# Optimization experiments

Hardware: AMD Instinct MI355X
Metric: run time of the kernel (lower is better)

## Reference

```python
import jax, jax.numpy as jnp
import numpy as np

EPS = 1e-6
GROUPS = 32  # min(C//4, 32) with C=256

def group_norm(x, scale, bias):
    B, H, W, C = x.shape
    g = GROUPS
    xg = x.reshape(B, H, W, g, C // g)
    mean = jnp.mean(xg, axis=(1, 2, 4), keepdims=True)
    var = jnp.var(xg, axis=(1, 2, 4), keepdims=True)
    xg = (xg - mean) * jax.lax.rsqrt(var + EPS)
    return xg.reshape(B, H, W, C) * scale + bias

def nin(x, w, b):
    return jnp.einsum('bhwc,cd->bhwd', x, w) + b

def setup_inputs() -> dict:
    key = jax.random.key(0)
    ks = jax.random.split(key, 11)
    B, H, W, C = 8, 64, 64, 256
    s = 1.0 / np.sqrt(C)
    return {
        'x': jax.random.normal(ks[0], (B, H, W, C), jnp.float32),
        'gn_scale': jnp.ones((C,), jnp.float32),
        'gn_bias': jnp.zeros((C,), jnp.float32),
        'Wq': jax.random.normal(ks[1], (C, C), jnp.float32) * s,
        'bq': jnp.zeros((C,), jnp.float32),
        'Wk': jax.random.normal(ks[2], (C, C), jnp.float32) * s,
        'bk': jnp.zeros((C,), jnp.float32),
        'Wv': jax.random.normal(ks[3], (C, C), jnp.float32) * s,
        'bv': jnp.zeros((C,), jnp.float32),
        'Wo': jax.random.normal(ks[4], (C, C), jnp.float32) * s * 0.1,
        'bo': jnp.zeros((C,), jnp.float32),
    }

def reference(x, gn_scale, gn_bias, Wq, bq, Wk, bk, Wv, bv, Wo, bo):
    B, H, W, C = x.shape
    h = group_norm(x, gn_scale, gn_bias)
    q = nin(h, Wq, bq)
    k = nin(h, Wk, bk)
    v = nin(h, Wv, bv)
    w = jnp.einsum('bhwc,bHWc->bhwHW', q, k) * (C ** -0.5)
    w = w.reshape(B, H, W, H * W)
    w = jax.nn.softmax(w, axis=-1)
    w = w.reshape(B, H, W, H, W)
    h = jnp.einsum('bhwHW,bHWc->bhwc', w, v)
    h = nin(h, Wo, bo)
    return x + h
```

## Files before the change

### kernel.cpp

```cpp
#include <hip/hip_runtime.h>
#include <stdint.h>

using short8 = __attribute__((ext_vector_type(8))) short;
using f32x4  = __attribute__((ext_vector_type(4))) float;

#define L2E 1.44269504088896f

static __device__ __forceinline__ unsigned short f2bf(float f) {
  union { float f; uint32_t u; } v; v.f = f;
  uint32_t r = v.u + 0x7fffu + ((v.u >> 16) & 1u);
  return (unsigned short)(r >> 16);
}
static __device__ __forceinline__ float bf2f(unsigned short u) {
  union { uint32_t u; float f; } v; v.u = ((uint32_t)u) << 16;
  return v.f;
}

static __device__ __forceinline__ void gload16(const unsigned short* g, unsigned short* l) {
  __builtin_amdgcn_global_load_lds(
      (const __attribute__((address_space(1))) void*)g,
      (__attribute__((address_space(3))) void*)l, 16, 0, 0);
}

static __device__ __forceinline__ float red_add_lg(float x) {
  x += __shfl_xor(x, 16);
  x += __shfl_xor(x, 32);
  return x;
}
static __device__ __forceinline__ float red_max_lg(float x) {
  x = fmaxf(x, __shfl_xor(x, 16));
  x = fmaxf(x, __shfl_xor(x, 32));
  return x;
}

__global__ __launch_bounds__(256) void prep_gn(
    const float* __restrict__ Wq, const float* __restrict__ Wk,
    const float* __restrict__ Wv, const float* __restrict__ Wo,
    const float* __restrict__ x,
    unsigned short* __restrict__ Wt, float* __restrict__ part) {
  int bid = blockIdx.x;
  int tid = threadIdx.x;
  if (bid < 1024) {
    int d = bid & 255, w = bid >> 8;
    const float* src = (w==0)?Wq:(w==1)?Wk:(w==2)?Wv:Wo;
    Wt[w*65536 + d*256 + tid] = f2bf(src[tid*256 + d]);
  } else {
    int v = bid - 1024;
    int ch = v & 63, b = v >> 6;
    float s = 0.f, q = 0.f;
    const float* p = x + ((b*4096) + ch*64)*256 + tid;
    for (int it = 0; it < 64; ++it) {
      float vv = p[it*256];
      s += vv; q += vv*vv;
    }
    s += __shfl_xor(s,1); q += __shfl_xor(q,1);
    s += __shfl_xor(s,2); q += __shfl_xor(q,2);
    s += __shfl_xor(s,4); q += __shfl_xor(q,4);
    if ((tid & 7) == 0) {
      int g = tid >> 3;
      part[((b*64 + ch)*32 + g)*2 + 0] = s;
      part[((b*64 + ch)*32 + g)*2 + 1] = q;
    }
  }
}

__global__ __launch_bounds__(256) void gn_apply(
    const float* __restrict__ x, const float* __restrict__ part,
    const float* __restrict__ sc, const float* __restrict__ bi,
    unsigned short* __restrict__ h) {
  int c = threadIdx.x, ch = blockIdx.x, b = blockIdx.y;
  int g = c >> 3;
  float s = 0.f, q = 0.f;
  for (int cc = 0; cc < 64; ++cc) {
    s += part[((b*64 + cc)*32 + g)*2 + 0];
    q += part[((b*64 + cc)*32 + g)*2 + 1];
  }
  float mean = s * (1.f/32768.f);
  float var  = q * (1.f/32768.f) - mean*mean;
  float rstd = rsqrtf(var + 1e-6f);
  float a  = rstd * sc[c];
  float d0 = bi[c] - mean * a;
  const float* p = x + ((b*4096) + ch*64)*256 + c;
  unsigned short* o = h + ((b*4096) + ch*64)*256 + c;
  for (int it = 0; it < 64; ++it)
    o[it*256] = f2bf(p[it*256] * a + d0);
}

__global__ __launch_bounds__(256) void gemm_qkvt(
    const unsigned short* __restrict__ A,
    const unsigned short* __restrict__ Wt,
    const float* __restrict__ bq,
    const float* __restrict__ bk,
    const float* __restrict__ bv,
    unsigned short* __restrict__ Qout,
    unsigned short* __restrict__ Kout,
    unsigned short* __restrict__ Vt) {
  int bid = blockIdx.x;
  int tid = threadIdx.x;
  int w = tid >> 6, l = tid & 63, lr = l & 15, lg = l >> 4;
  if (bid < 512) {
    const unsigned short* Wtq = Wt;
    const unsigned short* Wtk = Wt + 65536;
    int i0 = bid * 64;
    int j0 = w * 64;
    f32x4 accq[4][4] = {}, acck[4][4] = {};
#pragma unroll
    for (int kk = 0; kk < 8; ++kk) {
      short8 af[4], bfq[4], bfk[4];
#pragma unroll
      for (int mi = 0; mi < 4; ++mi)
        af[mi] = *(const short8*)(A + (i0 + mi*16 + lr)*256 + kk*32 + lg*8);
#pragma unroll
      for (int ni = 0; ni < 4; ++ni) {
        bfq[ni] = *(const short8*)(Wtq + (j0 + ni*16 + lr)*256 + kk*32 + lg*8);
        bfk[ni] = *(const short8*)(Wtk + (j0 + ni*16 + lr)*256 + kk*32 + lg*8);
      }
#pragma unroll
      for (int mi = 0; mi < 4; ++mi)
#pragma unroll
        for (int ni = 0; ni < 4; ++ni) {
          accq[mi][ni] = __builtin_amdgcn_mfma_f32_16x16x32_bf16(af[mi], bfq[ni], accq[mi][ni], 0,0,0);
          acck[mi][ni] = __builtin_amdgcn_mfma_f32_16x16x32_bf16(af[mi], bfk[ni], acck[mi][ni], 0,0,0);
        }
    }
#pragma unroll
    for (int mi = 0; mi < 4; ++mi) {
#pragma unroll
      for (int ni = 0; ni < 4; ++ni) {
        int j = j0 + ni*16 + lr;
#pragma unroll
        for (int r = 0; r < 4; ++r) {
          int i = i0 + mi*16 + lg*4 + r;
          Qout[i*256 + j] = f2bf((accq[mi][ni][r] + bq[j]) * 0.0625f);
          Kout[i*256 + j] = f2bf(acck[mi][ni][r] + bk[j]);
        }
      }
    }
  } else {
    const unsigned short* Wtv = Wt + 131072;
    int v = bid - 512;
    int i0 = (v & 3) * 64;
    int j0 = (v >> 2) * 256 + w * 64;
    f32x4 acc[4][4] = {};
#pragma unroll
    for (int kk = 0; kk < 8; ++kk) {
      short8 af[4], bfr[4];
#pragma unroll
      for (int mi = 0; mi < 4; ++mi)
        af[mi] = *(const short8*)(Wtv + (i0 + mi*16 + lr)*256 + kk*32 + lg*8);
#pragma unroll
      for (int ni = 0; ni < 4; ++ni)
        bfr[ni] = *(const short8*)(A + (j0 + ni*16 + lr)*256 + kk*32 + lg*8);
#pragma unroll
      for (int mi = 0; mi < 4; ++mi)
#pragma unroll
        for (int ni = 0; ni < 4; ++ni)
          acc[mi][ni] = __builtin_amdgcn_mfma_f32_16x16x32_bf16(af[mi], bfr[ni], acc[mi][ni], 0,0,0);
    }
#pragma unroll
    for (int mi = 0; mi < 4; ++mi) {
#pragma unroll
      for (int ni = 0; ni < 4; ++ni) {
        int j = j0 + ni*16 + lr;
#pragma unroll
        for (int r = 0; r < 4; ++r) {
          int i = i0 + mi*16 + lg*4 + r;
          int idx = ((j >> 12) << 20) + i*4096 + (j & 4095);
          Vt[idx] = f2bf(acc[mi][ni][r] + bv[i]);
        }
      }
    }
  }
}

__global__ __launch_bounds__(256) void gemm_bt(
    const unsigned short* __restrict__ A,
    const unsigned short* __restrict__ Bm,
    const float* __restrict__ bias_n,
    const float* __restrict__ resid,
    float* __restrict__ outp) {
  int tid = threadIdx.x;
  int w = tid >> 6, l = tid & 63, lr = l & 15, lg = l >> 4;
  int i0 = blockIdx.x * 64;
  int j0 = w * 64;
  f32x4 acc[4][4] = {};
#pragma unroll
  for (int kk = 0; kk < 8; ++kk) {
    short8 af[4], bfr[4];
#pragma unroll
    for (int mi = 0; mi < 4; ++mi)
      af[mi] = *(const short8*)(A + (i0 + mi*16 + lr)*256 + kk*32 + lg*8);
#pragma unroll
    for (int ni = 0; ni < 4; ++ni)
      bfr[ni] = *(const short8*)(Bm + (j0 + ni*16 + lr)*256 + kk*32 + lg*8);
#pragma unroll
    for (int mi = 0; mi < 4; ++mi)
#pragma unroll
      for (int ni = 0; ni < 4; ++ni)
        acc[mi][ni] = __builtin_amdgcn_mfma_f32_16x16x32_bf16(af[mi], bfr[ni], acc[mi][ni], 0,0,0);
  }
#pragma unroll
  for (int mi = 0; mi < 4; ++mi) {
#pragma unroll
    for (int ni = 0; ni < 4; ++ni) {
      int j = j0 + ni*16 + lr;
#pragma unroll
      for (int r = 0; r < 4; ++r) {
        int i = i0 + mi*16 + lg*4 + r;
        outp[i*256 + j] = acc[mi][ni][r] + bias_n[j] + resid[i*256 + j];
      }
    }
  }
}

__global__ __launch_bounds__(256) void gemm_fin(
    const unsigned short* __restrict__ P0,
    const unsigned short* __restrict__ P1,
    const float* __restrict__ stats,
    const unsigned short* __restrict__ Bm,
    const float* __restrict__ bias_n,
    const float* __restrict__ resid,
    float* __restrict__ outp) {
  int tid = threadIdx.x;
  int w = tid >> 6, l = tid & 63, lr = l & 15, lg = l >> 4;
  int i0 = blockIdx.x * 64;
  int j0 = w * 64;
  float a1m[4], a2m[4];
#pragma unroll
  for (int mi = 0; mi < 4; ++mi) {
    int row = i0 + mi*16 + lr;
    float m1 = stats[row*2 + 0],           l1 = stats[row*2 + 1];
    float m2 = stats[65536 + row*2 + 0],   l2 = stats[65536 + row*2 + 1];
    float M  = fmaxf(m1, m2);
    float a1 = __builtin_amdgcn_exp2f((m1 - M) * L2E);
    float a2 = __builtin_amdgcn_exp2f((m2 - M) * L2E);
    float inv = 1.f / (a1*l1 + a2*l2);
    a1m[mi] = a1 * inv; a2m[mi] = a2 * inv;
  }
  f32x4 acc[4][4] = {};
#pragma unroll
  for (int kk = 0; kk < 8; ++kk) {
    short8 af[4], bfr[4];
#pragma unroll
    for (int mi = 0; mi < 4; ++mi) {
      int off = (i0 + mi*16 + lr)*256 + kk*32 + lg*8;
      short8 v1 = *(const short8*)(P0 + off);
      short8 v2 = *(const short8*)(P1 + off);
      union { unsigned int u[4]; short8 s8; } pk;
#pragma unroll
      for (int e = 0; e < 4; ++e) {
        float g0 = bf2f((unsigned short)v1[2*e])   * a1m[mi] + bf2f((unsigned short)v2[2*e])   * a2m[mi];
        float g1 = bf2f((unsigned short)v1[2*e+1]) * a1m[mi] + bf2f((unsigned short)v2[2*e+1]) * a2m[mi];
        asm("v_cvt_pk_bf16_f32 %0, %1, %2" : "=v"(pk.u[e]) : "v"(g0), "v"(g1));
      }
      af[mi] = pk.s8;
    }
#pragma unroll
    for (int ni = 0; ni < 4; ++ni)
      bfr[ni] = *(const short8*)(Bm + (j0 + ni*16 + lr)*256 + kk*32 + lg*8);
#pragma unroll
    for (int mi = 0; mi < 4; ++mi)
#pragma unroll
      for (int ni = 0; ni < 4; ++ni)
        acc[mi][ni] = __builtin_amdgcn_mfma_f32_16x16x32_bf16(af[mi], bfr[ni], acc[mi][ni], 0,0,0);
  }
#pragma unroll
  for (int mi = 0; mi < 4; ++mi) {
#pragma unroll
    for (int ni = 0; ni < 4; ++ni) {
      int j = j0 + ni*16 + lr;
#pragma unroll
      for (int r = 0; r < 4; ++r) {
        int i = i0 + mi*16 + lg*4 + r;
        outp[i*256 + j] = acc[mi][ni][r] + bias_n[j] + resid[i*256 + j];
      }
    }
  }
}

static __device__ __forceinline__ void stage_kv32(
    const unsigned short* __restrict__ Kb, const unsigned short* __restrict__ Vb,
    int kt, unsigned short* dK, unsigned short* dV, int w, int l) {
#pragma unroll
  for (int i = 0; i < 4; ++i) {
    int t = (w*4 + i)*64 + l;
    int r = t >> 5, cs = t & 31;
    int cg = cs ^ (r & 7);
    gload16(Kb + (kt*32 + r)*256 + cg*8, dK + t*8);
  }
#pragma unroll
  for (int i = 0; i < 4; ++i) {
    int t = (w*4 + i)*64 + l;
    int d = t >> 2, s = t & 3;
    int sg = s ^ ((d ^ (d >> 2)) & 3);
    gload16(Vb + d*4096 + kt*32 + sg*8, dV + t*8);
  }
}

__global__ __launch_bounds__(256, 2) void attn_fwd(
    const unsigned short* __restrict__ Q,
    const unsigned short* __restrict__ Kmat,
    const unsigned short* __restrict__ Vt,
    unsigned short* __restrict__ P0,
    unsigned short* __restrict__ P1,
    float* __restrict__ stats) {
  __shared__ __align__(16) unsigned short ldsK[2][32][256];
  __shared__ __align__(16) unsigned short ldsV[2][256][32];

  int tid = threadIdx.x;
  int w = tid >> 6, l = tid & 63, lr = l & 15, lg = l >> 4;
  int b  = blockIdx.x & 7;
  int mt = (blockIdx.x >> 3) & 31;
  int ks = blockIdx.x >> 8;
  int m0 = mt*128 + w*32;
  int sw = lr & 7;
  int vsw = (lr ^ (lr >> 2)) & 3;
  int lgp = ((lg & 1) << 1) | (lg >> 1);

  const unsigned short* Kb = Kmat + b*(4096*256) + ks*(2048*256);
  const unsigned short* Vb = Vt   + (b << 20) + ks*2048;
  unsigned short* Pp = ks ? P1 : P0;

  short8 qf[2][8];
#pragma unroll
  for (int qn = 0; qn < 2; ++qn) {
    int qbase = ((b*4096) + m0 + qn*16 + lr)*256 + lg*8;
#pragma unroll
    for (int kk = 0; kk < 8; ++kk)
      qf[qn][kk] = *(const short8*)(Q + qbase + kk*32);
  }

  float mrun[2], lrun[2];
  f32x4 oacc[2][16] = {};
  mrun[0] = mrun[1] = -1e30f;
  lrun[0] = lrun[1] = 0.f;

  stage_kv32(Kb, Vb, 0, &ldsK[0][0][0], &ldsV[0][0][0], w, l);

  for (int kt = 0; kt < 64; ++kt) {
    int cur = kt & 1;
    if (kt < 63) {
      stage_kv32(Kb, Vb, kt+1, &ldsK[cur^1][0][0], &ldsV[cur^1][0][0], w, l);
      asm volatile("s_waitcnt vmcnt(8)" ::: "memory");
    } else {
      asm volatile("s_waitcnt vmcnt(0)" ::: "memory");
    }
    __builtin_amdgcn_s_barrier();
    __builtin_amdgcn_sched_barrier(0);

    const unsigned short (*Kc)[256] = ldsK[cur];
    const unsigned short (*Vc)[32]  = ldsV[cur];

    f32x4 s_[2][2];
#pragma unroll
    for (int qn = 0; qn < 2; ++qn)
#pragma unroll
      for (int kn = 0; kn < 2; ++kn) s_[qn][kn] = (f32x4){0.f,0.f,0.f,0.f};
#pragma unroll
    for (int kn = 0; kn < 2; ++kn) {
#pragma unroll
      for (int kk = 0; kk < 8; ++kk) {
        short8 kf = *(const short8*)&Kc[kn*16 + lr][((kk*4 + lg) ^ sw)*8];
        s_[0][kn] = __builtin_amdgcn_mfma_f32_16x16x32_bf16(kf, qf[0][kk], s_[0][kn], 0,0,0);
        s_[1][kn] = __builtin_amdgcn_mfma_f32_16x16x32_bf16(kf, qf[1][kk], s_[1][kn], 0,0,0);
      }
    }

    short8 pa[2];
#pragma unroll
    for (int qn = 0; qn < 2; ++qn) {
      float ma = fmaxf(fmaxf(s_[qn][0][0], s_[qn][0][1]), fmaxf(s_[qn][0][2], s_[qn][0][3]));
      float mb = fmaxf(fmaxf(s_[qn][1][0], s_[qn][1][1]), fmaxf(s_[qn][1][2], s_[qn][1][3]));
      float pmax = fmaxf(ma, mb);
      if (__any(pmax > mrun[qn] + 8.f)) {
        float mx = red_max_lg(pmax);
        float mnew = fmaxf(mrun[qn], mx);
        float alpha = __builtin_amdgcn_exp2f((mrun[qn] - mnew) * L2E);
        mrun[qn] = mnew;
        lrun[qn] *= alpha;
        float at[4];
#pragma unroll
        for (int r = 0; r < 4; ++r) at[r] = __shfl(alpha, lg*4 + r);
#pragma unroll
        for (int jt = 0; jt < 16; ++jt)
#pragma unroll
          for (int r = 0; r < 4; ++r) oacc[qn][jt][r] *= at[r];
      }
      float mL = mrun[qn] * L2E;
      float p[2][4];
#pragma unroll
      for (int kn = 0; kn < 2; ++kn)
#pragma unroll
        for (int r = 0; r < 4; ++r)
          p[kn][r] = __builtin_amdgcn_exp2f(s_[qn][kn][r]*L2E - mL);
      float t0 = (p[0][0]+p[0][1]) + (p[0][2]+p[0][3]);
      float t1 = (p[1][0]+p[1][1]) + (p[1][2]+p[1][3]);
      lrun[qn] += red_add_lg(t0 + t1);
      unsigned int X0, X1, Y0, Y1;
      asm("v_cvt_pk_bf16_f32 %0, %1, %2" : "=v"(X0) : "v"(p[0][0]), "v"(p[0][1]));
      asm("v_cvt_pk_bf16_f32 %0, %1, %2" : "=v"(X1) : "v"(p[0][2]), "v"(p[0][3]));
      asm("v_cvt_pk_bf16_f32 %0, %1, %2" : "=v"(Y0) : "v"(p[1][0]), "v"(p[1][1]));
      asm("v_cvt_pk_bf16_f32 %0, %1, %2" : "=v"(Y1) : "v"(p[1][2]), "v"(p[1][3]));
      asm("v_permlane16_swap_b32 %0, %1" : "+v"(X0), "+v"(Y0));
      asm("v_permlane16_swap_b32 %0, %1" : "+v"(X1), "+v"(Y1));
      union { unsigned int u[4]; short8 s8; } pk;
      pk.u[0] = X0; pk.u[1] = X1; pk.u[2] = Y0; pk.u[3] = Y1;
      pa[qn] = pk.s8;
    }

#pragma unroll
    for (int jt = 0; jt < 16; ++jt) {
      short8 vf = *(const short8*)&Vc[jt*16 + lr][(lgp ^ vsw)*8];
      oacc[0][jt] = __builtin_amdgcn_mfma_f32_16x16x32_bf16(pa[0], vf, oacc[0][jt], 0,0,0);
      oacc[1][jt] = __builtin_amdgcn_mfma_f32_16x16x32_bf16(pa[1], vf, oacc[1][jt], 0,0,0);
    }
    __builtin_amdgcn_sched_barrier(0);
    __builtin_amdgcn_s_barrier();
  }

  if (lg == 0) {
#pragma unroll
    for (int qn = 0; qn < 2; ++qn) {
      int row = b*4096 + m0 + qn*16 + lr;
      stats[(ks*32768 + row)*2 + 0] = mrun[qn];
      stats[(ks*32768 + row)*2 + 1] = lrun[qn];
    }
  }
#pragma unroll
  for (int qn = 0; qn < 2; ++qn) {
#pragma unroll
    for (int r = 0; r < 4; ++r) {
      int row = ((b*4096) + m0 + qn*16 + lg*4 + r)*256;
#pragma unroll
      for (int jt = 0; jt < 16; ++jt)
        Pp[row + jt*16 + lr] = f2bf(oacc[qn][jt][r]);
    }
  }
}

__global__ __launch_bounds__(256) void merge_attn(
    const unsigned short* __restrict__ P0,
    const unsigned short* __restrict__ P1,
    const float* __restrict__ stats,
    unsigned short* __restrict__ Out) {
  int tid = threadIdx.x;
  int row = blockIdx.x*8 + (tid >> 5);
  int c8  = (tid & 31) * 8;
  float m1 = stats[row*2 + 0],          l1 = stats[row*2 + 1];
  float m2 = stats[(32768 + row)*2 + 0], l2 = stats[(32768 + row)*2 + 1];
  float M  = fmaxf(m1, m2);
  float a1 = __builtin_amdgcn_exp2f((m1 - M) * L2E);
  float a2 = __builtin_amdgcn_exp2f((m2 - M) * L2E);
  float inv = 1.f / (a1*l1 + a2*l2);
  a1 *= inv; a2 *= inv;
  short8 v1 = *(const short8*)(P0 + row*256 + c8);
  short8 v2 = *(const short8*)(P1 + row*256 + c8);
  union { unsigned short u[8]; short8 s8; } o;
#pragma unroll
  for (int j = 0; j < 8; ++j)
    o.u[j] = f2bf(bf2f((unsigned short)v1[j])*a1 + bf2f((unsigned short)v2[j])*a2);
  *(short8*)(Out + row*256 + c8) = o.s8;
}

extern "C" void kernel_launch(void* const* d_in, const int* in_sizes, int n_in,
                              void* d_out, int out_size, void* d_ws, size_t ws_size,
                              hipStream_t stream) {
  (void)in_sizes; (void)n_in; (void)out_size;
  const float* x  = (const float*)d_in[0];
  const float* gs = (const float*)d_in[1];
  const float* gb = (const float*)d_in[2];
  const float* Wq = (const float*)d_in[3];
  const float* bq = (const float*)d_in[4];
  const float* Wk = (const float*)d_in[5];
  const float* bk = (const float*)d_in[6];
  const float* Wv = (const float*)d_in[7];
  const float* bv = (const float*)d_in[8];
  const float* Wo = (const float*)d_in[9];
  const float* bo = (const float*)d_in[10];

  char* ws = (char*)d_ws;
  unsigned short* h  = (unsigned short*)(ws);
  unsigned short* Qb = (unsigned short*)(ws + (size_t)16777216);
  unsigned short* Kb = (unsigned short*)(ws + (size_t)33554432);
  unsigned short* Vt = (unsigned short*)(ws + (size_t)50331648);
  unsigned short* Wt = (unsigned short*)(ws + (size_t)67108864);
  float* part        = (float*)(ws + (size_t)67633152);
  float* stats       = (float*)(ws + (size_t)67764224);
  unsigned short* P1ws = (unsigned short*)(ws + (size_t)68288512);
  bool fuse = (ws_size >= (size_t)68288512 + 16777216);
  unsigned short* Op1 = fuse ? P1ws : (unsigned short*)d_out;

  prep_gn <<<dim3(1536), 256, 0, stream>>>(Wq, Wk, Wv, Wo, x, Wt, part);
  gn_apply<<<dim3(64,8),  256, 0, stream>>>(x, part, gs, gb, h);
  gemm_qkvt<<<dim3(1024), 256, 0, stream>>>(h, Wt, bq, bk, bv, Qb, Kb, Vt);
  attn_fwd<<<dim3(512),  256, 0, stream>>>(Qb, Kb, Vt, h, Op1, stats);
  if (fuse) {
    gemm_fin<<<dim3(512), 256, 0, stream>>>(h, P1ws, stats, Wt+196608, bo, x, (float*)d_out);
  } else {
    merge_attn<<<dim3(4096), 256, 0, stream>>>(h, Op1, stats, Qb);
    gemm_bt<<<dim3(512), 256, 0, stream>>>(Qb, Wt+196608, bo, x, (float*)d_out);
  }
}
```

Before: 293.2 us.

## Switch attention kernel from 16x16x32 to 32x32x16 bf16 MFMA tiles

Rewrites the flash-attention inner loop so each wave handles its 32 query rows with one 32x32x16 MFMA accumulator for scores and eight 32x32 output accumulators, replacing the pairs of 16x16x32 tiles. The softmax row statistics now need only one cross-half shuffle, and P is repacked with permlane32_swap. The V LDS swizzle is changed to match the new read pattern. The larger MFMA shape is meant to cut the number of LDS fragment reads and MFMA issue overhead per tile, at the cost of a different register layout and the risk of new LDS bank conflicts.

```diff
diff --git a/kernel.cpp b/kernel.cpp
--- a/kernel.cpp
+++ b/kernel.cpp
@@ -3,6 +3,7 @@
 
 using short8 = __attribute__((ext_vector_type(8))) short;
 using f32x4  = __attribute__((ext_vector_type(4))) float;
+using f32x16 = __attribute__((ext_vector_type(16))) float;
 
 #define L2E 1.44269504088896f
 
@@ -20,17 +21,6 @@
   __builtin_amdgcn_global_load_lds(
       (const __attribute__((address_space(1))) void*)g,
       (__attribute__((address_space(3))) void*)l, 16, 0, 0);
-}
-
-static __device__ __forceinline__ float red_add_lg(float x) {
-  x += __shfl_xor(x, 16);
-  x += __shfl_xor(x, 32);
-  return x;
-}
-static __device__ __forceinline__ float red_max_lg(float x) {
-  x = fmaxf(x, __shfl_xor(x, 16));
-  x = fmaxf(x, __shfl_xor(x, 32));
-  return x;
 }
 
 __global__ __launch_bounds__(256) void prep_gn(
@@ -292,7 +282,7 @@
   for (int i = 0; i < 4; ++i) {
     int t = (w*4 + i)*64 + l;
     int d = t >> 2, s = t & 3;
-    int sg = s ^ ((d ^ (d >> 2)) & 3);
+    int sg = s ^ ((d >> 1) & 3);
     gload16(Vb + d*4096 + kt*32 + sg*8, dV + t*8);
   }
 }
@@ -308,32 +298,28 @@
   __shared__ __align__(16) unsigned short ldsV[2][256][32];
 
   int tid = threadIdx.x;
-  int w = tid >> 6, l = tid & 63, lr = l & 15, lg = l >> 4;
+  int w = tid >> 6, l = tid & 63, l31 = l & 31, hh = l >> 5;
   int b  = blockIdx.x & 7;
   int mt = (blockIdx.x >> 3) & 31;
   int ks = blockIdx.x >> 8;
   int m0 = mt*128 + w*32;
-  int sw = lr & 7;
-  int vsw = (lr ^ (lr >> 2)) & 3;
-  int lgp = ((lg & 1) << 1) | (lg >> 1);
+  int ksw = l31 & 7;
+  int vsw = (l31 >> 1) & 3;
 
   const unsigned short* Kb = Kmat + b*(4096*256) + ks*(2048*256);
   const unsigned short* Vb = Vt   + (b << 20) + ks*2048;
   unsigned short* Pp = ks ? P1 : P0;
 
-  short8 qf[2][8];
-#pragma unroll
-  for (int qn = 0; qn < 2; ++qn) {
-    int qbase = ((b*4096) + m0 + qn*16 + lr)*256 + lg*8;
-#pragma unroll
-    for (int kk = 0; kk < 8; ++kk)
-      qf[qn][kk] = *(const short8*)(Q + qbase + kk*32);
-  }
-
-  float mrun[2], lrun[2];
-  f32x4 oacc[2][16] = {};
-  mrun[0] = mrun[1] = -1e30f;
-  lrun[0] = lrun[1] = 0.f;
+  short8 qf[16];
+  {
+    int qbase = ((b*4096) + m0 + l31)*256 + hh*8;
+#pragma unroll
+    for (int kk = 0; kk < 16; ++kk)
+      qf[kk] = *(const short8*)(Q + qbase + kk*16);
+  }
+
+  float mrun = -1e30f, lrun = 0.f;
+  f32x16 oacc[8] = {};
 
   stage_kv32(Kb, Vb, 0, &ldsK[0][0][0], &ldsV[0][0][0], w, l);
 
@@ -351,89 +337,82 @@
     const unsigned short (*Kc)[256] = ldsK[cur];
     const unsigned short (*Vc)[32]  = ldsV[cur];
 
-    f32x4 s_[2][2];
-#pragma unroll
-    for (int qn = 0; qn < 2; ++qn)
-#pragma unroll
-      for (int kn = 0; kn < 2; ++kn) s_[qn][kn] = (f32x4){0.f,0.f,0.f,0.f};
-#pragma unroll
-    for (int kn = 0; kn < 2; ++kn) {
-#pragma unroll
-      for (int kk = 0; kk < 8; ++kk) {
-        short8 kf = *(const short8*)&Kc[kn*16 + lr][((kk*4 + lg) ^ sw)*8];
-        s_[0][kn] = __builtin_amdgcn_mfma_f32_16x16x32_bf16(kf, qf[0][kk], s_[0][kn], 0,0,0);
-        s_[1][kn] = __builtin_amdgcn_mfma_f32_16x16x32_bf16(kf, qf[1][kk], s_[1][kn], 0,0,0);
-      }
-    }
-
-    short8 pa[2];
-#pragma unroll
-    for (int qn = 0; qn < 2; ++qn) {
-      float ma = fmaxf(fmaxf(s_[qn][0][0], s_[qn][0][1]), fmaxf(s_[qn][0][2], s_[qn][0][3]));
-      float mb = fmaxf(fmaxf(s_[qn][1][0], s_[qn][1][1]), fmaxf(s_[qn][1][2], s_[qn][1][3]));
-      float pmax = fmaxf(ma, mb);
-      if (__any(pmax > mrun[qn] + 8.f)) {
-        float mx = red_max_lg(pmax);
-        float mnew = fmaxf(mrun[qn], mx);
-        float alpha = __builtin_amdgcn_exp2f((mrun[qn] - mnew) * L2E);
-        mrun[qn] = mnew;
-        lrun[qn] *= alpha;
-        float at[4];
-#pragma unroll
-        for (int r = 0; r < 4; ++r) at[r] = __shfl(alpha, lg*4 + r);
-#pragma unroll
-        for (int jt = 0; jt < 16; ++jt)
-#pragma unroll
-          for (int r = 0; r < 4; ++r) oacc[qn][jt][r] *= at[r];
-      }
-      float mL = mrun[qn] * L2E;
-      float p[2][4];
-#pragma unroll
-      for (int kn = 0; kn < 2; ++kn)
-#pragma unroll
-        for (int r = 0; r < 4; ++r)
-          p[kn][r] = __builtin_amdgcn_exp2f(s_[qn][kn][r]*L2E - mL);
-      float t0 = (p[0][0]+p[0][1]) + (p[0][2]+p[0][3]);
-      float t1 = (p[1][0]+p[1][1]) + (p[1][2]+p[1][3]);
-      lrun[qn] += red_add_lg(t0 + t1);
-      unsigned int X0, X1, Y0, Y1;
-      asm("v_cvt_pk_bf16_f32 %0, %1, %2" : "=v"(X0) : "v"(p[0][0]), "v"(p[0][1]));
-      asm("v_cvt_pk_bf16_f32 %0, %1, %2" : "=v"(X1) : "v"(p[0][2]), "v"(p[0][3]));
-      asm("v_cvt_pk_bf16_f32 %0, %1, %2" : "=v"(Y0) : "v"(p[1][0]), "v"(p[1][1]));
-      asm("v_cvt_pk_bf16_f32 %0, %1, %2" : "=v"(Y1) : "v"(p[1][2]), "v"(p[1][3]));
-      asm("v_permlane16_swap_b32 %0, %1" : "+v"(X0), "+v"(Y0));
-      asm("v_permlane16_swap_b32 %0, %1" : "+v"(X1), "+v"(Y1));
+    f32x16 s_ = {};
+#pragma unroll
+    for (int kk = 0; kk < 16; ++kk) {
+      short8 kf = *(const short8*)&Kc[l31][(((kk << 1) | hh) ^ ksw)*8];
+      s_ = __builtin_amdgcn_mfma_f32_32x32x16_bf16(kf, qf[kk], s_, 0,0,0);
+    }
+
+    float x0 = fmaxf(fmaxf(s_[0],s_[1]),   fmaxf(s_[2],s_[3]));
+    float x1 = fmaxf(fmaxf(s_[4],s_[5]),   fmaxf(s_[6],s_[7]));
+    float x2 = fmaxf(fmaxf(s_[8],s_[9]),   fmaxf(s_[10],s_[11]));
+    float x3 = fmaxf(fmaxf(s_[12],s_[13]), fmaxf(s_[14],s_[15]));
+    float pmax = fmaxf(fmaxf(x0,x1), fmaxf(x2,x3));
+    pmax = fmaxf(pmax, __shfl_xor(pmax, 32));
+    if (__any(pmax > mrun + 8.f)) {
+      float mnew = fmaxf(mrun, pmax);
+      float alpha = __builtin_amdgcn_exp2f((mrun - mnew) * L2E);
+      mrun = mnew;
+      lrun *= alpha;
+      float at[16];
+#pragma unroll
+      for (int r = 0; r < 16; ++r)
+        at[r] = __shfl(alpha, (l & 32) | ((r&3) + 8*(r>>2) + 4*hh));
+#pragma unroll
+      for (int jt = 0; jt < 8; ++jt)
+#pragma unroll
+        for (int r = 0; r < 16; ++r) oacc[jt][r] *= at[r];
+    }
+    float mL = mrun * L2E;
+    float p[16];
+#pragma unroll
+    for (int r = 0; r < 16; ++r)
+      p[r] = __builtin_amdgcn_exp2f(s_[r]*L2E - mL);
+    float t0 = ((p[0]+p[1]) + (p[2]+p[3])) + ((p[4]+p[5]) + (p[6]+p[7]));
+    float t1 = ((p[8]+p[9]) + (p[10]+p[11])) + ((p[12]+p[13]) + (p[14]+p[15]));
+    float sum = t0 + t1;
+    lrun += sum + __shfl_xor(sum, 32);
+
+    short8 paf[2];
+#pragma unroll
+    for (int kk2 = 0; kk2 < 2; ++kk2) {
+      int base = kk2*8;
+      unsigned int D0, D1, D2, D3;
+      asm("v_cvt_pk_bf16_f32 %0, %1, %2" : "=v"(D0) : "v"(p[base+0]), "v"(p[base+1]));
+      asm("v_cvt_pk_bf16_f32 %0, %1, %2" : "=v"(D1) : "v"(p[base+2]), "v"(p[base+3]));
+      asm("v_cvt_pk_bf16_f32 %0, %1, %2" : "=v"(D2) : "v"(p[base+4]), "v"(p[base+5]));
+      asm("v_cvt_pk_bf16_f32 %0, %1, %2" : "=v"(D3) : "v"(p[base+6]), "v"(p[base+7]));
+      asm("v_permlane32_swap_b32 %0, %1" : "+v"(D0), "+v"(D2));
+      asm("v_permlane32_swap_b32 %0, %1" : "+v"(D1), "+v"(D3));
       union { unsigned int u[4]; short8 s8; } pk;
-      pk.u[0] = X0; pk.u[1] = X1; pk.u[2] = Y0; pk.u[3] = Y1;
-      pa[qn] = pk.s8;
-    }
-
-#pragma unroll
-    for (int jt = 0; jt < 16; ++jt) {
-      short8 vf = *(const short8*)&Vc[jt*16 + lr][(lgp ^ vsw)*8];
-      oacc[0][jt] = __builtin_amdgcn_mfma_f32_16x16x32_bf16(pa[0], vf, oacc[0][jt], 0,0,0);
-      oacc[1][jt] = __builtin_amdgcn_mfma_f32_16x16x32_bf16(pa[1], vf, oacc[1][jt], 0,0,0);
+      pk.u[0] = D0; pk.u[1] = D1; pk.u[2] = D2; pk.u[3] = D3;
+      paf[kk2] = pk.s8;
+    }
+
+#pragma unroll
+    for (int kk2 = 0; kk2 < 2; ++kk2) {
+#pragma unroll
+      for (int jt = 0; jt < 8; ++jt) {
+        short8 vf = *(const short8*)&Vc[jt*32 + l31][(((kk2 << 1) | hh) ^ vsw)*8];
+        oacc[jt] = __builtin_amdgcn_mfma_f32_32x32x16_bf16(paf[kk2], vf, oacc[jt], 0,0,0);
+      }
     }
     __builtin_amdgcn_sched_barrier(0);
     __builtin_amdgcn_s_barrier();
   }
 
-  if (lg == 0) {
-#pragma unroll
-    for (int qn = 0; qn < 2; ++qn) {
-      int row = b*4096 + m0 + qn*16 + lr;
-      stats[(ks*32768 + row)*2 + 0] = mrun[qn];
-      stats[(ks*32768 + row)*2 + 1] = lrun[qn];
-    }
-  }
-#pragma unroll
-  for (int qn = 0; qn < 2; ++qn) {
-#pragma unroll
-    for (int r = 0; r < 4; ++r) {
-      int row = ((b*4096) + m0 + qn*16 + lg*4 + r)*256;
-#pragma unroll
-      for (int jt = 0; jt < 16; ++jt)
-        Pp[row + jt*16 + lr] = f2bf(oacc[qn][jt][r]);
+  if (l < 32) {
+    int row = b*4096 + m0 + l;
+    stats[(ks*32768 + row)*2 + 0] = mrun;
+    stats[(ks*32768 + row)*2 + 1] = lrun;
+  }
+#pragma unroll
+  for (int jt = 0; jt < 8; ++jt) {
+#pragma unroll
+    for (int r = 0; r < 16; ++r) {
+      int q = (r&3) + 8*(r>>2) + 4*hh;
+      Pp[((b*4096) + m0 + q)*256 + jt*32 + l31] = f2bf(oacc[jt][r]);
     }
   }
 }
```

Result: slower. 299.4 us (+2.1%).
